# Kernel tuning notes

Hardware: AMD Instinct MI355X
Metric: run time of the kernel (lower is better)

## Reference

```python
import jax, jax.numpy as jnp
import numpy as np

NEG_INF = -9e16
SLOPE = 0.2  # leaky relu slope


def setup_inputs() -> dict:
    key = jax.random.key(0)
    k1, k2, k3, k4 = jax.random.split(key, 4)
    N, F_in, H, D = 3072, 512, 8, 64
    h = jax.random.normal(k1, (N, F_in), dtype=jnp.float32)
    adj = jax.random.randint(k2, (N, N), 0, 2, dtype=jnp.int32)
    W = jax.random.normal(k3, (H, F_in, D), dtype=jnp.float32) * (2.0 / (F_in + D)) ** 0.5
    a = jax.random.normal(k4, (H, 2 * D, 1), dtype=jnp.float32) * (2.0 / (2 * D + 1)) ** 0.5
    return {"h": h, "adj": adj, "W": W, "a": a}


def reference(h, adj, W, a):
    # h: [N, F], W: [H, F, D], a: [H, 2D, 1], adj: [N, N]
    H, _, D = W.shape
    ht = jnp.einsum("nf,hfd->hnd", h, W)            # [H, N, D]
    a_src = a[:, :D, 0]                               # [H, D]
    a_dst = a[:, D:, 0]                               # [H, D]
    src = jnp.einsum("hnd,hd->hn", ht, a_src)        # [H, N]
    dst = jnp.einsum("hnd,hd->hn", ht, a_dst)        # [H, N]
    e = src[:, :, None] + dst[:, None, :]             # [H, N, N]
    e = jnp.where(e > 0, e, SLOPE * e)                # leaky relu
    e = jnp.where(adj[None] > 0, e, NEG_INF)
    att = jax.nn.softmax(e, axis=-1)                  # [H, N, N]
    hp = jnp.einsum("hnm,hmd->hnd", att, ht)         # [H, N, D]
    out = jnp.transpose(hp, (1, 0, 2)).reshape(h.shape[0], H * D)  # concat heads
    return (out, att)
```

## Files before the change

kernel.cpp:

```cpp
#include <hip/hip_runtime.h>

#define NN 3072
#define FF 512
#define HH 8
#define DD 64
#define SLOPEV 0.2f
#define CH2 64
#define NC2 (NN/CH2)

typedef __bf16  bf16x8 __attribute__((ext_vector_type(8)));
typedef __bf16  bf16x4 __attribute__((ext_vector_type(4)));
typedef short   s16x8  __attribute__((ext_vector_type(8)));
typedef float   f32x4  __attribute__((ext_vector_type(4)));
typedef unsigned long long u64;

#define MFMA16(a,b,c) __builtin_amdgcn_mfma_f32_16x16x32_bf16((a),(b),(c),0,0,0)

__device__ __forceinline__ short f2bf(float x){ __bf16 b=(__bf16)x; return __builtin_bit_cast(short,b); }
__device__ __forceinline__ float bf2f(short s){ return (float)__builtin_bit_cast(__bf16,s); }
__device__ __forceinline__ bf16x8 ldbf8(const short* p){ return __builtin_bit_cast(bf16x8, *(const s16x8*)p); }

__device__ __forceinline__ void gload16(const void* g, void* l){
  __builtin_amdgcn_global_load_lds(
      (const __attribute__((address_space(1))) void*)(uintptr_t)g,
      (__attribute__((address_space(3))) void*)(uint32_t)(uintptr_t)l, 16, 0, 0);
}

__global__ __launch_bounds__(256) void k_split_h(const float* __restrict__ h,
    short* __restrict__ hhi, short* __restrict__ hlo){
  size_t base = ((size_t)blockIdx.x*256 + threadIdx.x)*8;
  float4 v0 = *(const float4*)(h+base);
  float4 v1 = *(const float4*)(h+base+4);
  float vv[8] = {v0.x,v0.y,v0.z,v0.w,v1.x,v1.y,v1.z,v1.w};
  s16x8 hi, lo;
  #pragma unroll
  for (int j=0;j<8;j++){ short s=f2bf(vv[j]); hi[j]=s; lo[j]=f2bf(vv[j]-bf2f(s)); }
  *(s16x8*)(hhi+base)=hi; *(s16x8*)(hlo+base)=lo;
}

__global__ __launch_bounds__(64) void k_wt(const float* __restrict__ W, const float* __restrict__ a,
    short* __restrict__ wthi, short* __restrict__ wtlo,
    float* __restrict__ wasrc, float* __restrict__ wadst){
  int h = blockIdx.y, f0 = blockIdx.x*8, d = threadIdx.x;
  float asv = a[h*2*DD + d];
  float adv = a[h*2*DD + DD + d];
  s16x8 vh, vl;
  #pragma unroll
  for (int j=0;j<8;j++){
    float v = W[((size_t)h*FF + f0 + j)*DD + d];
    short s = f2bf(v); vh[j]=s; vl[j]=f2bf(v-bf2f(s));
    float ws_ = v*asv, wd_ = v*adv;
    #pragma unroll
    for (int m=1;m<64;m<<=1){ ws_ += __shfl_xor(ws_,m,64); wd_ += __shfl_xor(wd_,m,64); }
    if (d==0){ wasrc[h*FF+f0+j]=ws_; wadst[h*FF+f0+j]=wd_; }
  }
  size_t o = ((size_t)h*DD + d)*FF + f0;
  *(s16x8*)(wthi+o)=vh; *(s16x8*)(wtlo+o)=vl;
}

__global__ __launch_bounds__(256) void k_pack(const int* __restrict__ adj, u64* __restrict__ padj){
  int idx = blockIdx.x*256 + threadIdx.x;
  u64 b = __ballot(adj[idx] > 0);
  if ((threadIdx.x & 63) == 0) padj[idx>>6] = b;
}

__global__ __launch_bounds__(256) void k_srcdst(const float* __restrict__ h,
    const float* __restrict__ wasrc, const float* __restrict__ wadst,
    float* __restrict__ src, float* __restrict__ dst){
  int n = blockIdx.x*4 + (threadIdx.x>>6);
  int lane = threadIdx.x & 63;
  const float* hp = h + (size_t)n*FF + lane*8;
  float4 x0 = *(const float4*)hp, x1 = *(const float4*)(hp+4);
  float xs[8] = {x0.x,x0.y,x0.z,x0.w,x1.x,x1.y,x1.z,x1.w};
  float ps[HH], pd[HH];
  #pragma unroll
  for (int hh=0; hh<HH; hh++){
    const float* sp = wasrc + (size_t)hh*FF + lane*8;
    const float* dp = wadst + (size_t)hh*FF + lane*8;
    float4 s0 = *(const float4*)sp, s1 = *(const float4*)(sp+4);
    float4 t0 = *(const float4*)dp, t1 = *(const float4*)(dp+4);
    ps[hh] = xs[0]*s0.x + xs[1]*s0.y + xs[2]*s0.z + xs[3]*s0.w
           + xs[4]*s1.x + xs[5]*s1.y + xs[6]*s1.z + xs[7]*s1.w;
    pd[hh] = xs[0]*t0.x + xs[1]*t0.y + xs[2]*t0.z + xs[3]*t0.w
           + xs[4]*t1.x + xs[5]*t1.y + xs[6]*t1.z + xs[7]*t1.w;
  }
  #pragma unroll
  for (int m=1;m<64;m<<=1){
    #pragma unroll
    for (int hh=0; hh<HH; hh++){ ps[hh] += __shfl_xor(ps[hh],m,64); pd[hh] += __shfl_xor(pd[hh],m,64); }
  }
  if (lane==0){
    #pragma unroll
    for (int hh=0; hh<HH; hh++){ src[hh*NN+n]=ps[hh]; dst[hh*NN+n]=pd[hh]; }
  }
}

__global__ __launch_bounds__(256) void k_rowsum(const u64* __restrict__ padj,
    const float* __restrict__ src, const float* __restrict__ dst,
    float* __restrict__ rowsums){
  int wid = blockIdx.x*4 + (threadIdx.x>>6);
  int lane = threadIdx.x & 63;
  int h = wid / NN, n = wid - h*NN;
  float srcv = src[h*NN + n];
  const float* dsth = dst + h*NN;
  const u64* arow = padj + (size_t)n*(NN/64);
  float s = 0.f;
  #pragma unroll 4
  for (int i=0;i<NN/64;i++){
    u64 w = arow[i];
    float dv = dsth[i*64 + lane];
    float ev = srcv + dv;
    ev = fmaxf(ev, SLOPEV*ev);
    s += ((w >> lane) & 1ull) ? __expf(ev) : 0.f;
  }
  #pragma unroll
  for (int m=1;m<64;m<<=1) s += __shfl_xor(s, m, 64);
  if (lane == 0) rowsums[h*NN + n] = s;
}

__global__ __launch_bounds__(128) void k_ht(const short* __restrict__ hhi, const short* __restrict__ hlo,
    const short* __restrict__ wthi, const short* __restrict__ wtlo,
    short* __restrict__ hthi){
  __shared__ short tH[64][40];
  int h = blockIdx.y, n0 = blockIdx.x*32;
  int w = threadIdx.x>>6, lane = threadIdx.x&63;
  int r15 = lane&15, g = lane>>4;
  int arow = n0 + w*16 + r15;
  f32x4 acc[4] = {{0.f,0.f,0.f,0.f},{0.f,0.f,0.f,0.f},{0.f,0.f,0.f,0.f},{0.f,0.f,0.f,0.f}};
  const short* ha = hhi + (size_t)arow*FF + g*8;
  const short* la = hlo + (size_t)arow*FF + g*8;
  for (int kk=0; kk<FF; kk+=32){
    bf16x8 ahi = ldbf8(ha+kk), alo = ldbf8(la+kk);
    #pragma unroll
    for (int c=0;c<4;c++){
      size_t bo = ((size_t)h*DD + c*16 + r15)*FF + g*8 + kk;
      bf16x8 bh = ldbf8(wthi + bo), bl = ldbf8(wtlo + bo);
      acc[c] = MFMA16(ahi,bh,acc[c]);
      acc[c] = MFMA16(ahi,bl,acc[c]);
      acc[c] = MFMA16(alo,bh,acc[c]);
    }
  }
  #pragma unroll
  for (int c=0;c<4;c++){
    #pragma unroll
    for (int r=0;r<4;r++){
      int dloc = c*16 + r15, nloc = w*16 + g*4 + r;
      tH[dloc][nloc] = f2bf(acc[c][r]);
    }
  }
  __syncthreads();
  int row = threadIdx.x>>1, half = threadIdx.x&1;
  size_t o = ((size_t)h*DD + row)*NN + n0 + half*16;
  *(s16x8*)(hthi + o)     = *(const s16x8*)&tH[row][half*16];
  *(s16x8*)(hthi + o + 8) = *(const s16x8*)&tH[row][half*16+8];
}

__global__ __launch_bounds__(512, 8) void k_att(const u64* __restrict__ padj,
    const float* __restrict__ src, const float* __restrict__ dst,
    const float* __restrict__ rowsums,
    const short* __restrict__ hthi, float* __restrict__ dout){
  __shared__ short hA[64][CH2], hB[64][CH2];
  __shared__ short pA[32][CH2], pB[32][CH2];
  const size_t OUTOFF = (size_t)NN*HH*DD;
  int bid = blockIdx.x;
  int h = bid & 7, n0 = (bid >> 3) * 32;
  int t = threadIdx.x;
  int r = t>>4, j = t&15;
  int nrow = n0 + r;
  float srcv = src[h*NN + nrow];
  const float* dsth = dst + h*NN;
  const u64* arow = padj + (size_t)nrow*(NN/64);

  int wv = t>>6, lane = t&63, r15 = lane&15, g = lane>>4;
  int cblk = wv&3, nh = wv>>2;
  int drow = t>>3;
  int sslot = (t&7) ^ (drow&7);
  const short* gh = hthi + ((size_t)(h*DD) + drow)*NN + sslot*8;

  gload16(gh, &hA[wv*8][0]);

  float tot = rowsums[h*NN + nrow];
  float inv = (tot > 0.f) ? 1.f/tot : (1.f/(float)NN);
  bool am = !(tot > 0.f);

  f32x4 acc = {0.f,0.f,0.f,0.f};
  float* attrow = dout + OUTOFF + ((size_t)(h*NN + nrow))*NN;
  int aoff0 = (cblk*16 + r15)*(CH2*2);
  int boff0 = (nh*16 + r15)*(CH2*2);
  int csw   = (r15&7)<<4;
  int pofs  = r*(CH2*2) + ((j*8) ^ ((r&7)<<4));

  u64 bits = arow[0];
  const float* dvp = dsth + j*4;
  float4 dv = *(const float4*)dvp;

  #pragma unroll 2
  for (int c=0;c<NC2-1;c++){
    short (*hc)[CH2] = (c&1)?hB:hA;
    short (*hn)[CH2] = (c&1)?hA:hB;
    short (*pc)[CH2] = (c&1)?pB:pA;

    gload16(gh + (c+1)*CH2, &hn[wv*8][0]);
    u64 bits_n = arow[c+1];
    float4 dv_n = *(const float4*)(dvp + (c+1)*CH2);
    float o[4];
    #pragma unroll
    for (int e=0;e<4;e++){
      float ev = srcv + ((const float*)&dv)[e];
      ev = fmaxf(ev, SLOPEV*ev);
      float p = ((bits >> (j*4 + e)) & 1ull) ? __expf(ev) : 0.f;
      if (am) p = 1.f;
      o[e] = p * inv;
    }
    f32x4 s0 = {o[0],o[1],o[2],o[3]};
    __builtin_nontemporal_store(s0, (f32x4*)(attrow + c*CH2 + j*4));
    bf16x4 pb;
    #pragma unroll
    for (int e=0;e<4;e++) pb[e] = (__bf16)o[e];
    *(bf16x4*)((char*)pc + pofs) = pb;

    __builtin_amdgcn_sched_barrier(0);
    asm volatile("s_waitcnt vmcnt(4) lgkmcnt(0)" ::: "memory");
    __builtin_amdgcn_sched_barrier(0);
    __builtin_amdgcn_s_barrier();
    __builtin_amdgcn_sched_barrier(0);

    const char* hcB = (const char*)hc;
    const char* pcB = (const char*)pc;
    #pragma unroll
    for (int ks=0;ks<2;ks++){
      int kb = (g*16 + ks*64) ^ csw;
      bf16x8 bf = *(const bf16x8*)(pcB + boff0 + kb);
      bf16x8 ah = *(const bf16x8*)(hcB + aoff0 + kb);
      acc = MFMA16(ah, bf, acc);
    }
    asm volatile("" ::: "memory");
    __builtin_amdgcn_s_barrier();
    __builtin_amdgcn_sched_barrier(0);

    bits = bits_n; dv = dv_n;
  }

  {
    const int c = NC2-1;
    short (*hc)[CH2] = (c&1)?hB:hA;
    short (*pc)[CH2] = (c&1)?pB:pA;
    float o[4];
    #pragma unroll
    for (int e=0;e<4;e++){
      float ev = srcv + ((const float*)&dv)[e];
      ev = fmaxf(ev, SLOPEV*ev);
      float p = ((bits >> (j*4 + e)) & 1ull) ? __expf(ev) : 0.f;
      if (am) p = 1.f;
      o[e] = p * inv;
    }
    f32x4 s0 = {o[0],o[1],o[2],o[3]};
    __builtin_nontemporal_store(s0, (f32x4*)(attrow + c*CH2 + j*4));
    bf16x4 pb;
    #pragma unroll
    for (int e=0;e<4;e++) pb[e] = (__bf16)o[e];
    *(bf16x4*)((char*)pc + pofs) = pb;

    __builtin_amdgcn_sched_barrier(0);
    asm volatile("s_waitcnt vmcnt(4) lgkmcnt(0)" ::: "memory");
    __builtin_amdgcn_sched_barrier(0);
    __builtin_amdgcn_s_barrier();
    __builtin_amdgcn_sched_barrier(0);

    const char* hcB = (const char*)hc;
    const char* pcB = (const char*)pc;
    #pragma unroll
    for (int ks=0;ks<2;ks++){
      int kb = (g*16 + ks*64) ^ csw;
      bf16x8 bf = *(const bf16x8*)(pcB + boff0 + kb);
      bf16x8 ah = *(const bf16x8*)(hcB + aoff0 + kb);
      acc = MFMA16(ah, bf, acc);
    }
  }

  int n = n0 + nh*16 + r15;
  size_t ob = (size_t)n*(HH*DD) + h*DD + cblk*16 + g*4;
  __builtin_nontemporal_store(acc, (f32x4*)(dout+ob));
}

extern "C" void kernel_launch(void* const* d_in, const int* in_sizes, int n_in,
                              void* d_out, int out_size, void* d_ws, size_t ws_size,
                              hipStream_t stream) {
  const float* h   = (const float*)d_in[0];
  const int*   adj = (const int*)d_in[1];
  const float* W   = (const float*)d_in[2];
  const float* a   = (const float*)d_in[3];
  float* out = (float*)d_out;

  short* hhi  = (short*)d_ws;
  short* hlo  = hhi  + (size_t)NN*FF;
  short* wthi = hlo  + (size_t)NN*FF;
  short* wtlo = wthi + (size_t)HH*DD*FF;
  short* hthi = wtlo + (size_t)HH*DD*FF;
  float* wasrc= (float*)(hthi + (size_t)HH*DD*NN);
  float* wadst= wasrc + HH*FF;
  float* srcb = wadst + HH*FF;
  float* dstb = srcb + HH*NN;
  float* rsum = dstb + HH*NN;
  u64*   padj = (u64*)(rsum + HH*NN);

  k_split_h<<<dim3(NN*FF/(256*8)), 256, 0, stream>>>(h, hhi, hlo);
  k_wt     <<<dim3(FF/8, HH), 64, 0, stream>>>(W, a, wthi, wtlo, wasrc, wadst);
  k_pack   <<<dim3(NN*NN/256), 256, 0, stream>>>(adj, padj);
  k_srcdst <<<dim3(NN/4), 256, 0, stream>>>(h, wasrc, wadst, srcb, dstb);
  k_ht     <<<dim3(NN/32, HH), 128, 0, stream>>>(hhi, hlo, wthi, wtlo, hthi);
  k_rowsum <<<dim3(HH*NN/4), 256, 0, stream>>>(padj, srcb, dstb, rsum);
  k_att    <<<dim3(NN/32*HH), 512, 0, stream>>>(padj, srcb, dstb, rsum, hthi, out);
}
```

Before: 161.6 us.

## Split attention-matrix write into dedicated kernel and grid-stride adjacency packing

Moves the large fp32 attention matrix store out of the PV matmul kernel into a separate streaming kernel that recomputes the probabilities, so the MFMA loop carries no heavy global stores. The vmcnt waits are adjusted to match the removed stores, and the final output store becomes a plain store. The adjacency pack kernel now uses a fixed grid of 2048 blocks with a grid-stride loop. The split costs an extra pass that recomputes exp and rereads the packed adjacency and dst values, plus one more kernel launch.

Measured after the change: 196.4 us. 1.22x slower.

```diff
diff --git a/kernel.cpp b/kernel.cpp
--- a/kernel.cpp
+++ b/kernel.cpp
@@ -59,9 +59,11 @@
 }
 
 __global__ __launch_bounds__(256) void k_pack(const int* __restrict__ adj, u64* __restrict__ padj){
-  int idx = blockIdx.x*256 + threadIdx.x;
-  u64 b = __ballot(adj[idx] > 0);
-  if ((threadIdx.x & 63) == 0) padj[idx>>6] = b;
+  const int total = NN*NN;
+  for (int idx = blockIdx.x*256 + threadIdx.x; idx < total; idx += gridDim.x*256){
+    u64 b = __ballot(adj[idx] > 0);
+    if ((threadIdx.x & 63) == 0) padj[idx>>6] = b;
+  }
 }
 
 __global__ __launch_bounds__(256) void k_srcdst(const float* __restrict__ h,
@@ -155,13 +157,12 @@
   *(s16x8*)(hthi + o + 8) = *(const s16x8*)&tH[row][half*16+8];
 }
 
-__global__ __launch_bounds__(512, 8) void k_att(const u64* __restrict__ padj,
+__global__ __launch_bounds__(512, 8) void k_pv(const u64* __restrict__ padj,
     const float* __restrict__ src, const float* __restrict__ dst,
     const float* __restrict__ rowsums,
     const short* __restrict__ hthi, float* __restrict__ dout){
   __shared__ short hA[64][CH2], hB[64][CH2];
   __shared__ short pA[32][CH2], pB[32][CH2];
-  const size_t OUTOFF = (size_t)NN*HH*DD;
   int bid = blockIdx.x;
   int h = bid & 7, n0 = (bid >> 3) * 32;
   int t = threadIdx.x;
@@ -184,7 +185,6 @@
   bool am = !(tot > 0.f);
 
   f32x4 acc = {0.f,0.f,0.f,0.f};
-  float* attrow = dout + OUTOFF + ((size_t)(h*NN + nrow))*NN;
   int aoff0 = (cblk*16 + r15)*(CH2*2);
   int boff0 = (nh*16 + r15)*(CH2*2);
   int csw   = (r15&7)<<4;
@@ -203,6 +203,7 @@
     gload16(gh + (c+1)*CH2, &hn[wv*8][0]);
     u64 bits_n = arow[c+1];
     float4 dv_n = *(const float4*)(dvp + (c+1)*CH2);
+
     float o[4];
     #pragma unroll
     for (int e=0;e<4;e++){
@@ -212,15 +213,13 @@
       if (am) p = 1.f;
       o[e] = p * inv;
     }
-    f32x4 s0 = {o[0],o[1],o[2],o[3]};
-    __builtin_nontemporal_store(s0, (f32x4*)(attrow + c*CH2 + j*4));
     bf16x4 pb;
     #pragma unroll
     for (int e=0;e<4;e++) pb[e] = (__bf16)o[e];
     *(bf16x4*)((char*)pc + pofs) = pb;
 
     __builtin_amdgcn_sched_barrier(0);
-    asm volatile("s_waitcnt vmcnt(4) lgkmcnt(0)" ::: "memory");
+    asm volatile("s_waitcnt vmcnt(5) lgkmcnt(0)" ::: "memory");
     __builtin_amdgcn_sched_barrier(0);
     __builtin_amdgcn_s_barrier();
     __builtin_amdgcn_sched_barrier(0);
@@ -254,15 +253,13 @@
       if (am) p = 1.f;
       o[e] = p * inv;
     }
-    f32x4 s0 = {o[0],o[1],o[2],o[3]};
-    __builtin_nontemporal_store(s0, (f32x4*)(attrow + c*CH2 + j*4));
     bf16x4 pb;
     #pragma unroll
     for (int e=0;e<4;e++) pb[e] = (__bf16)o[e];
     *(bf16x4*)((char*)pc + pofs) = pb;
 
     __builtin_amdgcn_sched_barrier(0);
-    asm volatile("s_waitcnt vmcnt(4) lgkmcnt(0)" ::: "memory");
+    asm volatile("s_waitcnt vmcnt(0) lgkmcnt(0)" ::: "memory");
     __builtin_amdgcn_sched_barrier(0);
     __builtin_amdgcn_s_barrier();
     __builtin_amdgcn_sched_barrier(0);
@@ -280,7 +277,46 @@
 
   int n = n0 + nh*16 + r15;
   size_t ob = (size_t)n*(HH*DD) + h*DD + cblk*16 + g*4;
-  __builtin_nontemporal_store(acc, (f32x4*)(dout+ob));
+  *(f32x4*)(dout+ob) = acc;
+}
+
+__global__ __launch_bounds__(512) void k_att_write(const u64* __restrict__ padj,
+    const float* __restrict__ src, const float* __restrict__ dst,
+    const float* __restrict__ rowsums, float* __restrict__ dout){
+  const size_t OUTOFF = (size_t)NN*HH*DD;
+  int wv = threadIdx.x>>6, lane = threadIdx.x&63;
+  int base_row = (blockIdx.x*8 + wv)*4;
+  int widx = lane>>4, sh = (lane&15)*4;
+  #pragma unroll
+  for (int k=0;k<4;k++){
+    int row = base_row + k;
+    int h = row / NN;
+    int n = row - h*NN;
+    float srcv = src[row];
+    float tot = rowsums[row];
+    float inv = (tot > 0.f) ? 1.f/tot : (1.f/(float)NN);
+    bool am = !(tot > 0.f);
+    const float* dsth = dst + h*NN;
+    const u64* arow = padj + (size_t)n*(NN/64);
+    float* attrow = dout + OUTOFF + (size_t)row*NN;
+    #pragma unroll 4
+    for (int i=0;i<NN/256;i++){
+      u64 w = arow[i*4 + widx];
+      const float* dp = dsth + i*256 + lane*4;
+      float4 dv = *(const float4*)dp;
+      float dj[4] = {dv.x, dv.y, dv.z, dv.w};
+      f32x4 o;
+      #pragma unroll
+      for (int e=0;e<4;e++){
+        float ev = srcv + dj[e];
+        ev = fmaxf(ev, SLOPEV*ev);
+        float p = ((w >> (sh+e)) & 1ull) ? __expf(ev) : 0.f;
+        if (am) p = 1.f;
+        o[e] = p * inv;
+      }
+      *(f32x4*)(attrow + i*256 + lane*4) = o;
+    }
+  }
 }
 
 extern "C" void kernel_launch(void* const* d_in, const int* in_sizes, int n_in,
@@ -304,11 +340,12 @@
   float* rsum = dstb + HH*NN;
   u64*   padj = (u64*)(rsum + HH*NN);
 
-  k_split_h<<<dim3(NN*FF/(256*8)), 256, 0, stream>>>(h, hhi, hlo);
-  k_wt     <<<dim3(FF/8, HH), 64, 0, stream>>>(W, a, wthi, wtlo, wasrc, wadst);
-  k_pack   <<<dim3(NN*NN/256), 256, 0, stream>>>(adj, padj);
-  k_srcdst <<<dim3(NN/4), 256, 0, stream>>>(h, wasrc, wadst, srcb, dstb);
-  k_ht     <<<dim3(NN/32, HH), 128, 0, stream>>>(hhi, hlo, wthi, wtlo, hthi);
-  k_rowsum <<<dim3(HH*NN/4), 256, 0, stream>>>(padj, srcb, dstb, rsum);
-  k_att    <<<dim3(NN/32*HH), 512, 0, stream>>>(padj, srcb, dstb, rsum, hthi, out);
-}
+  k_split_h  <<<dim3(NN*FF/(256*8)), 256, 0, stream>>>(h, hhi, hlo);
+  k_wt       <<<dim3(FF/8, HH), 64, 0, stream>>>(W, a, wthi, wtlo, wasrc, wadst);
+  k_pack     <<<dim3(2048), 256, 0, stream>>>(adj, padj);
+  k_srcdst   <<<dim3(NN/4), 256, 0, stream>>>(h, wasrc, wadst, srcb, dstb);
+  k_ht       <<<dim3(NN/32, HH), 128, 0, stream>>>(hhi, hlo, wthi, wtlo, hthi);
+  k_rowsum   <<<dim3(HH*NN/4), 256, 0, stream>>>(padj, srcb, dstb, rsum);
+  k_pv       <<<dim3(NN/32*HH), 512, 0, stream>>>(padj, srcb, dstb, rsum, hthi, out);
+  k_att_write<<<dim3(HH*NN/32), 512, 0, stream>>>(padj, srcb, dstb, rsum, out);
+}
```
